# Kernel optimization log

Hardware: AMD Instinct MI355X
Metric: run time of the kernel (lower is better)

Reference implementation:

```python
import jax, jax.numpy as jnp
import numpy as np

N_HEADS = 16
HEAD_SIZE = 64
SEQ_LEN = 2048
EMBED = 1024
BATCH = 2


def setup_inputs() -> dict:
    key = jax.random.key(0)
    ks = jax.random.split(key, 9)
    d_inner = N_HEADS * HEAD_SIZE
    s = 1.0 / np.sqrt(EMBED)
    inp = {
        "inputs": jax.random.normal(ks[0], (BATCH, SEQ_LEN, EMBED), jnp.float32),
        "Wq": jax.random.uniform(ks[1], (EMBED, d_inner), jnp.float32, -s, s),
        "bq": jax.random.uniform(ks[2], (d_inner,), jnp.float32, -s, s),
        "Wk": jax.random.uniform(ks[3], (EMBED, d_inner), jnp.float32, -s, s),
        "bk": jax.random.uniform(ks[4], (d_inner,), jnp.float32, -s, s),
        "Wv": jax.random.uniform(ks[5], (EMBED, d_inner), jnp.float32, -s, s),
        "bv": jax.random.uniform(ks[6], (d_inner,), jnp.float32, -s, s),
        "Wo": jax.random.uniform(ks[7], (d_inner, EMBED), jnp.float32, -s, s),
        "bo": jax.random.uniform(ks[8], (EMBED,), jnp.float32, -s, s),
    }
    return inp


def reference(inputs, Wq, bq, Wk, bk, Wv, bv, Wo, bo):
    B, S, _ = inputs.shape
    # QKV projections -> [B, H, S, Dh]
    def proj(W, b):
        return (inputs @ W + b).reshape(B, S, N_HEADS, HEAD_SIZE).transpose(0, 2, 1, 3)
    q, k, v = proj(Wq, bq), proj(Wk, bk), proj(Wv, bv)
    scores = jnp.einsum("bhqd,bhkd->bhqk", q, k) / jnp.sqrt(jnp.float32(HEAD_SIZE))
    causal = jnp.tril(jnp.ones((S, S), dtype=bool))  # [S, S]
    scores = jnp.where(causal[None, None], scores, -jnp.inf)
    attn = jax.nn.softmax(scores, axis=-1)  # dropout is identity in eval
    out = jnp.einsum("bhqk,bhkd->bhqd", attn, v)
    out = out.transpose(0, 2, 1, 3).reshape(B, S, N_HEADS * HEAD_SIZE)
    return out @ Wo + bo
```

## Files before the change

### kernel.cpp

```cpp
#include <hip/hip_runtime.h>
#include <hip/hip_bf16.h>
#include <math.h>

#define NH 16
#define DH 64
#define SEQ 2048
#define EMBED 1024
#define DINNER 1024
#define BATCH 2
#define MTOK 4096

typedef __bf16 bf16x8 __attribute__((ext_vector_type(8)));
typedef float  f32x4  __attribute__((ext_vector_type(4)));
typedef float  f32x16 __attribute__((ext_vector_type(16)));
typedef unsigned int u32;

__device__ __forceinline__ void gload16(const void* g, void* l) {
    __builtin_amdgcn_global_load_lds((const __attribute__((address_space(1))) void*)g,
                                     (__attribute__((address_space(3))) void*)l, 16, 0, 0);
}

__global__ __launch_bounds__(256) void cvt_bf16(
    const float* __restrict__ src, __bf16* __restrict__ dst, int n)
{
    int i = (blockIdx.x * 256 + threadIdx.x) * 4;
    if (i + 3 < n) {
        float4 v = *(const float4*)&src[i];
        dst[i + 0] = (__bf16)v.x;
        dst[i + 1] = (__bf16)v.y;
        dst[i + 2] = (__bf16)v.z;
        dst[i + 3] = (__bf16)v.w;
    }
}

__global__ __launch_bounds__(256) void tconv4(
    const float* __restrict__ W0, const float* __restrict__ W1,
    const float* __restrict__ W2, const float* __restrict__ W3,
    __bf16* __restrict__ D0, __bf16* __restrict__ D1,
    __bf16* __restrict__ D2, __bf16* __restrict__ D3)
{
    const int z = blockIdx.z;
    const float* __restrict__ src = (z == 0) ? W0 : (z == 1) ? W1 : (z == 2) ? W2 : W3;
    __bf16* __restrict__ dst      = (z == 0) ? D0 : (z == 1) ? D1 : (z == 2) ? D2 : D3;
    const int R = 1024, C = 1024;

    __shared__ float t[32][33];
    const int c0 = blockIdx.x * 32, r0 = blockIdx.y * 32;
    const int x = threadIdx.x & 31, y = threadIdx.x >> 5;
#pragma unroll
    for (int i = 0; i < 4; ++i)
        t[y + 8 * i][x] = src[(size_t)(r0 + y + 8 * i) * C + c0 + x];
    __syncthreads();
#pragma unroll
    for (int i = 0; i < 4; ++i)
        dst[(size_t)(c0 + y + 8 * i) * R + r0 + x] = (__bf16)t[x][y + 8 * i];
}

#define QSCALE 0.18033688f

__global__ __launch_bounds__(256) void gemm128(
    const __bf16* __restrict__ A,
    const __bf16* __restrict__ Bt0, const __bf16* __restrict__ Bt1, const __bf16* __restrict__ Bt2,
    const float* __restrict__ b0, const float* __restrict__ b1, const float* __restrict__ b2,
    void* __restrict__ o0, void* __restrict__ o1, void* __restrict__ o2,
    int Kdim, int mode3)
{
    const int z = blockIdx.z;
    const __bf16* __restrict__ Bt = (z == 0) ? Bt0 : (z == 1) ? Bt1 : Bt2;
    const float*  __restrict__ bias = (z == 0) ? b0 : (z == 1) ? b1 : b2;
    void* __restrict__ outp = (z == 0) ? o0 : (z == 1) ? o1 : o2;
    const int mode = mode3 ? 3 : z;
    const float scale = (mode == 0) ? QSCALE : 1.0f;

    __shared__ __bf16 As[128 * 32];
    __shared__ __bf16 Bs[128 * 32];

    const int tid  = threadIdx.x;
    const int lane = tid & 63;
    const int wid  = tid >> 6;
    const int wm = wid >> 1, wn = wid & 1;
    const int ls = lane & 15, lg = lane >> 4;
    const int m0 = blockIdx.y * 128, n0 = blockIdx.x * 128;

    const int sr = tid >> 2;
    const int sc = (tid & 3) * 8;

    f32x4 acc[4][4] = {};

    for (int k0 = 0; k0 < Kdim; k0 += 32) {
        gload16(&A [(size_t)(m0 + sr)      * Kdim + k0 + sc], &As[sr * 32 + sc]);
        gload16(&A [(size_t)(m0 + 64 + sr) * Kdim + k0 + sc], &As[(64 + sr) * 32 + sc]);
        gload16(&Bt[(size_t)(n0 + sr)      * Kdim + k0 + sc], &Bs[sr * 32 + sc]);
        gload16(&Bt[(size_t)(n0 + 64 + sr) * Kdim + k0 + sc], &Bs[(64 + sr) * 32 + sc]);
        __syncthreads();

        bf16x8 af[4], bfr[4];
#pragma unroll
        for (int i = 0; i < 4; ++i) {
            af[i]  = *(const bf16x8*)&As[(wm * 64 + i * 16 + ls) * 32 + lg * 8];
            bfr[i] = *(const bf16x8*)&Bs[(wn * 64 + i * 16 + ls) * 32 + lg * 8];
        }
#pragma unroll
        for (int i = 0; i < 4; ++i)
#pragma unroll
            for (int jx = 0; jx < 4; ++jx)
                acc[i][jx] = __builtin_amdgcn_mfma_f32_16x16x32_bf16(af[i], bfr[jx], acc[i][jx], 0, 0, 0);
        __syncthreads();
    }

#pragma unroll
    for (int i = 0; i < 4; ++i) {
#pragma unroll
        for (int jx = 0; jx < 4; ++jx) {
#pragma unroll
            for (int j = 0; j < 4; ++j) {
                const int m = m0 + wm * 64 + i * 16 + lg * 4 + j;
                const int n = n0 + wn * 64 + jx * 16 + ls;
                const float v = (acc[i][jx][j] + bias[n]) * scale;
                if (mode == 3) {
                    ((float*)outp)[(size_t)m * EMBED + n] = v;
                } else {
                    const int b = m >> 11, s = m & 2047;
                    const int h = n >> 6,  d = n & 63;
                    if (mode == 2)
                        ((__bf16*)outp)[(((size_t)(b * NH + h) * DH + d) << 11) + s] = (__bf16)v;
                    else
                        ((__bf16*)outp)[((((size_t)(b * NH + h) << 11) + s) * DH) + d] = (__bf16)v;
                }
            }
        }
    }
}

__global__ __launch_bounds__(128) void attn_mfma(
    const __bf16* __restrict__ Q, const __bf16* __restrict__ K,
    const __bf16* __restrict__ Vt, __bf16* __restrict__ ctx)
{
    __shared__ __bf16 lds[2][8192];

    const int tid  = threadIdx.x;
    const int wave = tid >> 6;
    const int lane = tid & 63;
    const int col  = lane & 31;
    const int hi   = lane >> 5;
    const int bh = blockIdx.x & 31;
    const int qt = 31 - (blockIdx.x >> 5);
    const int qb  = qt * 64;
    const int qlo = qb + wave * 32;
    const int b = bh >> 4, h = bh & 15;

    const __bf16* __restrict__ Qb = Q + ((size_t)bh << 11) * DH;
    const char* __restrict__ Kg = (const char*)(K  + ((size_t)bh << 11) * DH);
    const char* __restrict__ Vg = (const char*)(Vt + ((size_t)bh << 11) * DH);

    const int srow = tid >> 3;
    const int sswz = ((tid & 7) * 16) ^ ((srow & 7) << 4);

    bf16x8 qf[4];
#pragma unroll
    for (int c = 0; c < 4; ++c)
        qf[c] = *(const bf16x8*)&Qb[(size_t)(qlo + col) * DH + c * 16 + hi * 8];

    const int nt = qt + 1;

#pragma unroll
    for (int i = 0; i < 4; ++i) {
        const int row = i * 16 + srow;
        gload16(Kg + (size_t)row * 128 + sswz,
                (char*)&lds[0][0] + i * 2048 + tid * 16);
        gload16(Vg + (size_t)row * 4096 + sswz,
                (char*)&lds[0][0] + 8192 + i * 2048 + tid * 16);
    }
    __syncthreads();

    f32x16 oT0 = {}, oT1 = {};
    float mrun = -INFINITY, lrun = 0.f;
    int cur = 0;
    const int swz = (col & 7) << 4;

    for (int t = 0; t < nt; ++t) {
        if (t + 1 < nt) {
            const int kbn = (t + 1) * 64;
#pragma unroll
            for (int i = 0; i < 4; ++i) {
                const int row = i * 16 + srow;
                gload16(Kg + (size_t)(kbn + row) * 128 + sswz,
                        (char*)&lds[cur ^ 1][0] + i * 2048 + tid * 16);
                gload16(Vg + (size_t)row * 4096 + (size_t)kbn * 2 + sswz,
                        (char*)&lds[cur ^ 1][0] + 8192 + i * 2048 + tid * 16);
            }
        }

        const int k0 = t * 64;
        const char* ldsK = (const char*)&lds[cur][0];
        const char* ldsV = ldsK + 8192;

        bf16x8 kfa[4], kfb[4];
#pragma unroll
        for (int c = 0; c < 4; ++c) {
            kfa[c] = *(const bf16x8*)(ldsK + (     col) * 128 + ((c * 32 + hi * 16) ^ swz));
            kfb[c] = *(const bf16x8*)(ldsK + (32 + col) * 128 + ((c * 32 + hi * 16) ^ swz));
        }

        f32x16 sta = {}, stb = {};
#pragma unroll
        for (int c = 0; c < 4; ++c) {
            sta = __builtin_amdgcn_mfma_f32_32x32x16_bf16(kfa[c], qf[c], sta, 0, 0, 0);
            stb = __builtin_amdgcn_mfma_f32_32x32x16_bf16(kfb[c], qf[c], stb, 0, 0, 0);
        }

        if (k0 + 63 > qlo) {
#pragma unroll
            for (int r = 0; r < 16; ++r) {
                const int krel = (r & 3) + 8 * (r >> 2) + 4 * hi;
                if (k0 + krel > qlo + col)      sta[r] = -INFINITY;
                if (k0 + 32 + krel > qlo + col) stb[r] = -INFINITY;
            }
        }

        float ta = fmaxf(fmaxf(fmaxf(sta[0], sta[1]), fmaxf(sta[2], sta[3])),
                         fmaxf(fmaxf(sta[4], sta[5]), fmaxf(sta[6], sta[7])));
        float tb = fmaxf(fmaxf(fmaxf(sta[8], sta[9]),  fmaxf(sta[10], sta[11])),
                         fmaxf(fmaxf(sta[12], sta[13]), fmaxf(sta[14], sta[15])));
        float tc = fmaxf(fmaxf(fmaxf(stb[0], stb[1]), fmaxf(stb[2], stb[3])),
                         fmaxf(fmaxf(stb[4], stb[5]), fmaxf(stb[6], stb[7])));
        float td = fmaxf(fmaxf(fmaxf(stb[8], stb[9]),  fmaxf(stb[10], stb[11])),
                         fmaxf(fmaxf(stb[12], stb[13]), fmaxf(stb[14], stb[15])));
        float tmax = fmaxf(fmaxf(ta, tb), fmaxf(tc, td));
        tmax = fmaxf(tmax, __shfl_xor(tmax, 32));

        if (__any(tmax > mrun + 8.f)) {
            const float mnew = fmaxf(mrun, tmax);
            const float corr = exp2f(mrun - mnew);
            lrun *= corr;
            oT0 *= corr;
            oT1 *= corr;
            mrun = mnew;
        }

        float pa[16], pb[16];
#pragma unroll
        for (int r = 0; r < 16; ++r) { pa[r] = exp2f(sta[r] - mrun); pb[r] = exp2f(stb[r] - mrun); }
        float psa = (((pa[0] + pa[1]) + (pa[2] + pa[3])) + ((pa[4] + pa[5]) + (pa[6] + pa[7])))
                  + (((pa[8] + pa[9]) + (pa[10] + pa[11])) + ((pa[12] + pa[13]) + (pa[14] + pa[15])));
        float psb = (((pb[0] + pb[1]) + (pb[2] + pb[3])) + ((pb[4] + pb[5]) + (pb[6] + pb[7])))
                  + (((pb[8] + pb[9]) + (pb[10] + pb[11])) + ((pb[12] + pb[13]) + (pb[14] + pb[15])));
        float psum = psa + psb;
        psum += __shfl_xor(psum, 32);
        lrun += psum;

        u32 wa[8], wb[8];
#pragma unroll
        for (int i = 0; i < 8; ++i) {
            u32 r1, r2;
            asm("v_cvt_pk_bf16_f32 %0, %1, %2" : "=v"(r1) : "v"(pa[2 * i]), "v"(pa[2 * i + 1]));
            asm("v_cvt_pk_bf16_f32 %0, %1, %2" : "=v"(r2) : "v"(pb[2 * i]), "v"(pb[2 * i + 1]));
            wa[i] = r1; wb[i] = r2;
        }
        asm("v_permlane32_swap_b32 %0, %1" : "+v"(wa[0]), "+v"(wa[2]));
        asm("v_permlane32_swap_b32 %0, %1" : "+v"(wa[1]), "+v"(wa[3]));
        asm("v_permlane32_swap_b32 %0, %1" : "+v"(wa[4]), "+v"(wa[6]));
        asm("v_permlane32_swap_b32 %0, %1" : "+v"(wa[5]), "+v"(wa[7]));
        asm("v_permlane32_swap_b32 %0, %1" : "+v"(wb[0]), "+v"(wb[2]));
        asm("v_permlane32_swap_b32 %0, %1" : "+v"(wb[1]), "+v"(wb[3]));
        asm("v_permlane32_swap_b32 %0, %1" : "+v"(wb[4]), "+v"(wb[6]));
        asm("v_permlane32_swap_b32 %0, %1" : "+v"(wb[5]), "+v"(wb[7]));

        union { u32 u[4]; bf16x8 v; } cA0, cA1, cB0, cB1;
        cA0.u[0] = wa[0]; cA0.u[1] = wa[1]; cA0.u[2] = wa[2]; cA0.u[3] = wa[3];
        cA1.u[0] = wa[4]; cA1.u[1] = wa[5]; cA1.u[2] = wa[6]; cA1.u[3] = wa[7];
        cB0.u[0] = wb[0]; cB0.u[1] = wb[1]; cB0.u[2] = wb[2]; cB0.u[3] = wb[3];
        cB1.u[0] = wb[4]; cB1.u[1] = wb[5]; cB1.u[2] = wb[6]; cB1.u[3] = wb[7];

#pragma unroll
        for (int dh = 0; dh < 2; ++dh) {
            bf16x8 v0 = *(const bf16x8*)(ldsV + (dh * 32 + col) * 128 + ((0  + hi * 16) ^ swz));
            bf16x8 v1 = *(const bf16x8*)(ldsV + (dh * 32 + col) * 128 + ((32 + hi * 16) ^ swz));
            bf16x8 v2 = *(const bf16x8*)(ldsV + (dh * 32 + col) * 128 + ((64 + hi * 16) ^ swz));
            bf16x8 v3 = *(const bf16x8*)(ldsV + (dh * 32 + col) * 128 + ((96 + hi * 16) ^ swz));
            f32x16& o = dh ? oT1 : oT0;
            o = __builtin_amdgcn_mfma_f32_32x32x16_bf16(v0, cA0.v, o, 0, 0, 0);
            o = __builtin_amdgcn_mfma_f32_32x32x16_bf16(v1, cA1.v, o, 0, 0, 0);
            o = __builtin_amdgcn_mfma_f32_32x32x16_bf16(v2, cB0.v, o, 0, 0, 0);
            o = __builtin_amdgcn_mfma_f32_32x32x16_bf16(v3, cB1.v, o, 0, 0, 0);
        }

        __syncthreads();
        cur ^= 1;
    }

    const float inv = 1.0f / lrun;
    const size_t base = ((size_t)(b * SEQ + qlo + col)) * DINNER + h * 64;
#pragma unroll
    for (int g = 0; g < 4; ++g) {
        __bf16 t4[4];
#pragma unroll
        for (int j = 0; j < 4; ++j) t4[j] = (__bf16)(oT0[4 * g + j] * inv);
        *(uint2*)&ctx[base + 8 * g + 4 * hi] = *(uint2*)t4;
#pragma unroll
        for (int j = 0; j < 4; ++j) t4[j] = (__bf16)(oT1[4 * g + j] * inv);
        *(uint2*)&ctx[base + 32 + 8 * g + 4 * hi] = *(uint2*)t4;
    }
}

extern "C" void kernel_launch(void* const* d_in, const int* in_sizes, int n_in,
                              void* d_out, int out_size, void* d_ws, size_t ws_size,
                              hipStream_t stream)
{
    const float* X  = (const float*)d_in[0];
    const float* Wq = (const float*)d_in[1];
    const float* bq = (const float*)d_in[2];
    const float* Wk = (const float*)d_in[3];
    const float* bk = (const float*)d_in[4];
    const float* Wv = (const float*)d_in[5];
    const float* bv = (const float*)d_in[6];
    const float* Wo = (const float*)d_in[7];
    const float* bo = (const float*)d_in[8];
    float* out = (float*)d_out;

    __bf16* ws  = (__bf16*)d_ws;
    const size_t MI = 1048576;
    __bf16* Xb   = ws;
    __bf16* Wtq  = ws + 4  * MI;
    __bf16* Wtk  = ws + 5  * MI;
    __bf16* Wtv  = ws + 6  * MI;
    __bf16* Wto  = ws + 7  * MI;
    __bf16* Qb   = ws + 8  * MI;
    __bf16* Kb   = ws + 12 * MI;
    __bf16* Vtb  = ws + 16 * MI;
    __bf16* ctxb = ws + 20 * MI;

    cvt_bf16<<<dim3(MTOK * EMBED / 1024), dim3(256), 0, stream>>>(X, Xb, MTOK * EMBED);
    tconv4<<<dim3(32, 32, 4), dim3(256), 0, stream>>>(Wq, Wk, Wv, Wo, Wtq, Wtk, Wtv, Wto);

    {
        dim3 grid(DINNER / 128, MTOK / 128, 3), blk(256);
        gemm128<<<grid, blk, 0, stream>>>(Xb, Wtq, Wtk, Wtv, bq, bk, bv,
                                          Qb, Kb, Vtb, EMBED, 0);
    }

    {
        dim3 grid(32 * (SEQ / 64)), blk(128);
        attn_mfma<<<grid, blk, 0, stream>>>(Qb, Kb, Vtb, ctxb);
    }

    {
        dim3 grid(EMBED / 128, MTOK / 128, 1), blk(256);
        gemm128<<<grid, blk, 0, stream>>>(ctxb, Wto, Wto, Wto, bo, bo, bo,
                                          out, out, out, DINNER, 1);
    }
}
```

Before: 150.3 us.

## Split attention KV loop across two waves per 32-row query tile

Each block now handles a 32-row query tile instead of 64, and its two waves take alternating 64-key tiles of the causal KV range (split-K). At the end, the two waves' partial softmax states are merged through LDS using max/sum rescaling. The grid doubles to raise parallelism and balance work across the causal triangle. In exchange, K/V tiles are loaded per block for only 32 queries, which halves data reuse, and there is an extra LDS merge and sync while one wave sits idle during each tile.

```diff
diff --git a/kernel.cpp b/kernel.cpp
--- a/kernel.cpp
+++ b/kernel.cpp
@@ -143,10 +143,9 @@
     const int lane = tid & 63;
     const int col  = lane & 31;
     const int hi   = lane >> 5;
-    const int bh = blockIdx.x & 31;
-    const int qt = 31 - (blockIdx.x >> 5);
-    const int qb  = qt * 64;
-    const int qlo = qb + wave * 32;
+    const int bh   = blockIdx.x & 31;
+    const int qt32 = 63 - (blockIdx.x >> 5);
+    const int qlo  = qt32 * 32;
     const int b = bh >> 4, h = bh & 15;
 
     const __bf16* __restrict__ Qb = Q + ((size_t)bh << 11) * DH;
@@ -155,13 +154,14 @@
 
     const int srow = tid >> 3;
     const int sswz = ((tid & 7) * 16) ^ ((srow & 7) << 4);
+    const int swz  = (col & 7) << 4;
 
     bf16x8 qf[4];
 #pragma unroll
     for (int c = 0; c < 4; ++c)
         qf[c] = *(const bf16x8*)&Qb[(size_t)(qlo + col) * DH + c * 16 + hi * 8];
 
-    const int nt = qt + 1;
+    const int nt = (qt32 + 2) >> 1;
 
 #pragma unroll
     for (int i = 0; i < 4; ++i) {
@@ -176,7 +176,6 @@
     f32x16 oT0 = {}, oT1 = {};
     float mrun = -INFINITY, lrun = 0.f;
     int cur = 0;
-    const int swz = (col & 7) << 4;
 
     for (int t = 0; t < nt; ++t) {
         if (t + 1 < nt) {
@@ -191,115 +190,137 @@
             }
         }
 
-        const int k0 = t * 64;
-        const char* ldsK = (const char*)&lds[cur][0];
-        const char* ldsV = ldsK + 8192;
-
-        bf16x8 kfa[4], kfb[4];
-#pragma unroll
-        for (int c = 0; c < 4; ++c) {
-            kfa[c] = *(const bf16x8*)(ldsK + (     col) * 128 + ((c * 32 + hi * 16) ^ swz));
-            kfb[c] = *(const bf16x8*)(ldsK + (32 + col) * 128 + ((c * 32 + hi * 16) ^ swz));
-        }
-
-        f32x16 sta = {}, stb = {};
-#pragma unroll
-        for (int c = 0; c < 4; ++c) {
-            sta = __builtin_amdgcn_mfma_f32_32x32x16_bf16(kfa[c], qf[c], sta, 0, 0, 0);
-            stb = __builtin_amdgcn_mfma_f32_32x32x16_bf16(kfb[c], qf[c], stb, 0, 0, 0);
-        }
-
-        if (k0 + 63 > qlo) {
-#pragma unroll
-            for (int r = 0; r < 16; ++r) {
-                const int krel = (r & 3) + 8 * (r >> 2) + 4 * hi;
-                if (k0 + krel > qlo + col)      sta[r] = -INFINITY;
-                if (k0 + 32 + krel > qlo + col) stb[r] = -INFINITY;
-            }
-        }
-
-        float ta = fmaxf(fmaxf(fmaxf(sta[0], sta[1]), fmaxf(sta[2], sta[3])),
-                         fmaxf(fmaxf(sta[4], sta[5]), fmaxf(sta[6], sta[7])));
-        float tb = fmaxf(fmaxf(fmaxf(sta[8], sta[9]),  fmaxf(sta[10], sta[11])),
-                         fmaxf(fmaxf(sta[12], sta[13]), fmaxf(sta[14], sta[15])));
-        float tc = fmaxf(fmaxf(fmaxf(stb[0], stb[1]), fmaxf(stb[2], stb[3])),
-                         fmaxf(fmaxf(stb[4], stb[5]), fmaxf(stb[6], stb[7])));
-        float td = fmaxf(fmaxf(fmaxf(stb[8], stb[9]),  fmaxf(stb[10], stb[11])),
-                         fmaxf(fmaxf(stb[12], stb[13]), fmaxf(stb[14], stb[15])));
-        float tmax = fmaxf(fmaxf(ta, tb), fmaxf(tc, td));
-        tmax = fmaxf(tmax, __shfl_xor(tmax, 32));
-
-        if (__any(tmax > mrun + 8.f)) {
-            const float mnew = fmaxf(mrun, tmax);
-            const float corr = exp2f(mrun - mnew);
-            lrun *= corr;
-            oT0 *= corr;
-            oT1 *= corr;
-            mrun = mnew;
-        }
-
-        float pa[16], pb[16];
-#pragma unroll
-        for (int r = 0; r < 16; ++r) { pa[r] = exp2f(sta[r] - mrun); pb[r] = exp2f(stb[r] - mrun); }
-        float psa = (((pa[0] + pa[1]) + (pa[2] + pa[3])) + ((pa[4] + pa[5]) + (pa[6] + pa[7])))
-                  + (((pa[8] + pa[9]) + (pa[10] + pa[11])) + ((pa[12] + pa[13]) + (pa[14] + pa[15])));
-        float psb = (((pb[0] + pb[1]) + (pb[2] + pb[3])) + ((pb[4] + pb[5]) + (pb[6] + pb[7])))
-                  + (((pb[8] + pb[9]) + (pb[10] + pb[11])) + ((pb[12] + pb[13]) + (pb[14] + pb[15])));
-        float psum = psa + psb;
-        psum += __shfl_xor(psum, 32);
-        lrun += psum;
-
-        u32 wa[8], wb[8];
-#pragma unroll
-        for (int i = 0; i < 8; ++i) {
-            u32 r1, r2;
-            asm("v_cvt_pk_bf16_f32 %0, %1, %2" : "=v"(r1) : "v"(pa[2 * i]), "v"(pa[2 * i + 1]));
-            asm("v_cvt_pk_bf16_f32 %0, %1, %2" : "=v"(r2) : "v"(pb[2 * i]), "v"(pb[2 * i + 1]));
-            wa[i] = r1; wb[i] = r2;
-        }
-        asm("v_permlane32_swap_b32 %0, %1" : "+v"(wa[0]), "+v"(wa[2]));
-        asm("v_permlane32_swap_b32 %0, %1" : "+v"(wa[1]), "+v"(wa[3]));
-        asm("v_permlane32_swap_b32 %0, %1" : "+v"(wa[4]), "+v"(wa[6]));
-        asm("v_permlane32_swap_b32 %0, %1" : "+v"(wa[5]), "+v"(wa[7]));
-        asm("v_permlane32_swap_b32 %0, %1" : "+v"(wb[0]), "+v"(wb[2]));
-        asm("v_permlane32_swap_b32 %0, %1" : "+v"(wb[1]), "+v"(wb[3]));
-        asm("v_permlane32_swap_b32 %0, %1" : "+v"(wb[4]), "+v"(wb[6]));
-        asm("v_permlane32_swap_b32 %0, %1" : "+v"(wb[5]), "+v"(wb[7]));
-
-        union { u32 u[4]; bf16x8 v; } cA0, cA1, cB0, cB1;
-        cA0.u[0] = wa[0]; cA0.u[1] = wa[1]; cA0.u[2] = wa[2]; cA0.u[3] = wa[3];
-        cA1.u[0] = wa[4]; cA1.u[1] = wa[5]; cA1.u[2] = wa[6]; cA1.u[3] = wa[7];
-        cB0.u[0] = wb[0]; cB0.u[1] = wb[1]; cB0.u[2] = wb[2]; cB0.u[3] = wb[3];
-        cB1.u[0] = wb[4]; cB1.u[1] = wb[5]; cB1.u[2] = wb[6]; cB1.u[3] = wb[7];
-
-#pragma unroll
-        for (int dh = 0; dh < 2; ++dh) {
-            bf16x8 v0 = *(const bf16x8*)(ldsV + (dh * 32 + col) * 128 + ((0  + hi * 16) ^ swz));
-            bf16x8 v1 = *(const bf16x8*)(ldsV + (dh * 32 + col) * 128 + ((32 + hi * 16) ^ swz));
-            bf16x8 v2 = *(const bf16x8*)(ldsV + (dh * 32 + col) * 128 + ((64 + hi * 16) ^ swz));
-            bf16x8 v3 = *(const bf16x8*)(ldsV + (dh * 32 + col) * 128 + ((96 + hi * 16) ^ swz));
-            f32x16& o = dh ? oT1 : oT0;
-            o = __builtin_amdgcn_mfma_f32_32x32x16_bf16(v0, cA0.v, o, 0, 0, 0);
-            o = __builtin_amdgcn_mfma_f32_32x32x16_bf16(v1, cA1.v, o, 0, 0, 0);
-            o = __builtin_amdgcn_mfma_f32_32x32x16_bf16(v2, cB0.v, o, 0, 0, 0);
-            o = __builtin_amdgcn_mfma_f32_32x32x16_bf16(v3, cB1.v, o, 0, 0, 0);
+        if ((t & 1) == wave) {
+            const int k0 = t * 64;
+            const char* ldsK = (const char*)&lds[cur][0];
+            const char* ldsV = ldsK + 8192;
+
+            bf16x8 kfa[4], kfb[4];
+#pragma unroll
+            for (int c = 0; c < 4; ++c) {
+                kfa[c] = *(const bf16x8*)(ldsK + (     col) * 128 + ((c * 32 + hi * 16) ^ swz));
+                kfb[c] = *(const bf16x8*)(ldsK + (32 + col) * 128 + ((c * 32 + hi * 16) ^ swz));
+            }
+
+            f32x16 sta = {}, stb = {};
+#pragma unroll
+            for (int c = 0; c < 4; ++c) {
+                sta = __builtin_amdgcn_mfma_f32_32x32x16_bf16(kfa[c], qf[c], sta, 0, 0, 0);
+                stb = __builtin_amdgcn_mfma_f32_32x32x16_bf16(kfb[c], qf[c], stb, 0, 0, 0);
+            }
+
+            if (k0 + 63 > qlo) {
+#pragma unroll
+                for (int r = 0; r < 16; ++r) {
+                    const int krel = (r & 3) + 8 * (r >> 2) + 4 * hi;
+                    if (k0 + krel > qlo + col)      sta[r] = -INFINITY;
+                    if (k0 + 32 + krel > qlo + col) stb[r] = -INFINITY;
+                }
+            }
+
+            float ta = fmaxf(fmaxf(fmaxf(sta[0], sta[1]), fmaxf(sta[2], sta[3])),
+                             fmaxf(fmaxf(sta[4], sta[5]), fmaxf(sta[6], sta[7])));
+            float tb = fmaxf(fmaxf(fmaxf(sta[8], sta[9]),  fmaxf(sta[10], sta[11])),
+                             fmaxf(fmaxf(sta[12], sta[13]), fmaxf(sta[14], sta[15])));
+            float tc = fmaxf(fmaxf(fmaxf(stb[0], stb[1]), fmaxf(stb[2], stb[3])),
+                             fmaxf(fmaxf(stb[4], stb[5]), fmaxf(stb[6], stb[7])));
+            float td = fmaxf(fmaxf(fmaxf(stb[8], stb[9]),  fmaxf(stb[10], stb[11])),
+                             fmaxf(fmaxf(stb[12], stb[13]), fmaxf(stb[14], stb[15])));
+            float tmax = fmaxf(fmaxf(ta, tb), fmaxf(tc, td));
+            tmax = fmaxf(tmax, __shfl_xor(tmax, 32));
+
+            if (__any(tmax > mrun + 8.f)) {
+                const float mnew = fmaxf(mrun, tmax);
+                const float corr = exp2f(mrun - mnew);
+                lrun *= corr;
+                oT0 *= corr;
+                oT1 *= corr;
+                mrun = mnew;
+            }
+
+            float pa[16], pb[16];
+#pragma unroll
+            for (int r = 0; r < 16; ++r) { pa[r] = exp2f(sta[r] - mrun); pb[r] = exp2f(stb[r] - mrun); }
+            float psa = (((pa[0] + pa[1]) + (pa[2] + pa[3])) + ((pa[4] + pa[5]) + (pa[6] + pa[7])))
+                      + (((pa[8] + pa[9]) + (pa[10] + pa[11])) + ((pa[12] + pa[13]) + (pa[14] + pa[15])));
+            float psb = (((pb[0] + pb[1]) + (pb[2] + pb[3])) + ((pb[4] + pb[5]) + (pb[6] + pb[7])))
+                      + (((pb[8] + pb[9]) + (pb[10] + pb[11])) + ((pb[12] + pb[13]) + (pb[14] + pb[15])));
+            float psum = psa + psb;
+            psum += __shfl_xor(psum, 32);
+            lrun += psum;
+
+            u32 wa[8], wb[8];
+#pragma unroll
+            for (int i = 0; i < 8; ++i) {
+                u32 r1, r2;
+                asm("v_cvt_pk_bf16_f32 %0, %1, %2" : "=v"(r1) : "v"(pa[2 * i]), "v"(pa[2 * i + 1]));
+                asm("v_cvt_pk_bf16_f32 %0, %1, %2" : "=v"(r2) : "v"(pb[2 * i]), "v"(pb[2 * i + 1]));
+                wa[i] = r1; wb[i] = r2;
+            }
+            asm("v_permlane32_swap_b32 %0, %1" : "+v"(wa[0]), "+v"(wa[2]));
+            asm("v_permlane32_swap_b32 %0, %1" : "+v"(wa[1]), "+v"(wa[3]));
+            asm("v_permlane32_swap_b32 %0, %1" : "+v"(wa[4]), "+v"(wa[6]));
+            asm("v_permlane32_swap_b32 %0, %1" : "+v"(wa[5]), "+v"(wa[7]));
+            asm("v_permlane32_swap_b32 %0, %1" : "+v"(wb[0]), "+v"(wb[2]));
+            asm("v_permlane32_swap_b32 %0, %1" : "+v"(wb[1]), "+v"(wb[3]));
+            asm("v_permlane32_swap_b32 %0, %1" : "+v"(wb[4]), "+v"(wb[6]));
+            asm("v_permlane32_swap_b32 %0, %1" : "+v"(wb[5]), "+v"(wb[7]));
+
+            union { u32 u4[4]; bf16x8 v; } cA0, cA1, cB0, cB1;
+            cA0.u4[0] = wa[0]; cA0.u4[1] = wa[1]; cA0.u4[2] = wa[2]; cA0.u4[3] = wa[3];
+            cA1.u4[0] = wa[4]; cA1.u4[1] = wa[5]; cA1.u4[2] = wa[6]; cA1.u4[3] = wa[7];
+            cB0.u4[0] = wb[0]; cB0.u4[1] = wb[1]; cB0.u4[2] = wb[2]; cB0.u4[3] = wb[3];
+            cB1.u4[0] = wb[4]; cB1.u4[1] = wb[5]; cB1.u4[2] = wb[6]; cB1.u4[3] = wb[7];
+
+#pragma unroll
+            for (int dh = 0; dh < 2; ++dh) {
+                bf16x8 v0 = *(const bf16x8*)(ldsV + (dh * 32 + col) * 128 + ((0  + hi * 16) ^ swz));
+                bf16x8 v1 = *(const bf16x8*)(ldsV + (dh * 32 + col) * 128 + ((32 + hi * 16) ^ swz));
+                bf16x8 v2 = *(const bf16x8*)(ldsV + (dh * 32 + col) * 128 + ((64 + hi * 16) ^ swz));
+                bf16x8 v3 = *(const bf16x8*)(ldsV + (dh * 32 + col) * 128 + ((96 + hi * 16) ^ swz));
+                f32x16& o = dh ? oT1 : oT0;
+                o = __builtin_amdgcn_mfma_f32_32x32x16_bf16(v0, cA0.v, o, 0, 0, 0);
+                o = __builtin_amdgcn_mfma_f32_32x32x16_bf16(v1, cA1.v, o, 0, 0, 0);
+                o = __builtin_amdgcn_mfma_f32_32x32x16_bf16(v2, cB0.v, o, 0, 0, 0);
+                o = __builtin_amdgcn_mfma_f32_32x32x16_bf16(v3, cB1.v, o, 0, 0, 0);
+            }
         }
 
         __syncthreads();
         cur ^= 1;
     }
 
-    const float inv = 1.0f / lrun;
-    const size_t base = ((size_t)(b * SEQ + qlo + col)) * DINNER + h * 64;
-#pragma unroll
-    for (int g = 0; g < 4; ++g) {
-        __bf16 t4[4];
-#pragma unroll
-        for (int j = 0; j < 4; ++j) t4[j] = (__bf16)(oT0[4 * g + j] * inv);
-        *(uint2*)&ctx[base + 8 * g + 4 * hi] = *(uint2*)t4;
-#pragma unroll
-        for (int j = 0; j < 4; ++j) t4[j] = (__bf16)(oT1[4 * g + j] * inv);
-        *(uint2*)&ctx[base + 32 + 8 * g + 4 * hi] = *(uint2*)t4;
+    float* mrg = (float*)&lds[0][0];
+    if (wave == 1) {
+#pragma unroll
+        for (int r = 0; r < 16; ++r) {
+            mrg[r * 64 + lane]        = oT0[r];
+            mrg[(16 + r) * 64 + lane] = oT1[r];
+        }
+        mrg[32 * 64 + lane] = mrun;
+        mrg[33 * 64 + lane] = lrun;
+    }
+    __syncthreads();
+    if (wave == 0) {
+        const float m1 = mrg[32 * 64 + lane];
+        const float l1 = mrg[33 * 64 + lane];
+        const float M  = fmaxf(mrun, m1);
+        const float c0 = exp2f(mrun - M);
+        const float c1 = (m1 == -INFINITY) ? 0.f : exp2f(m1 - M);
+        const float inv = 1.0f / (lrun * c0 + l1 * c1);
+        const size_t base = ((size_t)(b * SEQ + qlo + col)) * DINNER + h * 64;
+#pragma unroll
+        for (int g = 0; g < 4; ++g) {
+            __bf16 t4[4];
+#pragma unroll
+            for (int j = 0; j < 4; ++j)
+                t4[j] = (__bf16)((oT0[4 * g + j] * c0 + mrg[(4 * g + j) * 64 + lane] * c1) * inv);
+            *(uint2*)&ctx[base + 8 * g + 4 * hi] = *(uint2*)t4;
+#pragma unroll
+            for (int j = 0; j < 4; ++j)
+                t4[j] = (__bf16)((oT1[4 * g + j] * c0 + mrg[(16 + 4 * g + j) * 64 + lane] * c1) * inv);
+            *(uint2*)&ctx[base + 32 + 8 * g + 4 * hi] = *(uint2*)t4;
+        }
     }
 }
 
@@ -340,7 +361,7 @@
     }
 
     {
-        dim3 grid(32 * (SEQ / 64)), blk(128);
+        dim3 grid(32 * (SEQ / 32)), blk(128);
         attn_mfma<<<grid, blk, 0, stream>>>(Qb, Kb, Vtb, ctxb);
     }
 
```

Result: no change. 151.6 us (+0.9%).

## Use single-wave attention blocks with split K/V single-buffer prefetch and waitcnt sync

Applied to the files above, without the earlier changes.

Each attention workgroup now holds one wave covering 32 queries instead of two waves covering 64, which doubles the grid and removes __syncthreads. The double-buffered LDS is replaced by a single buffer. The next K tile is prefetched after the QK MFMAs and the next V tile after the PV MFMAs, with explicit vmcnt/lgkmcnt waits and setprio around the MFMA sections. This aims to cut LDS use and barrier cost and improve occupancy. In exchange, each wave now loads its own K/V tiles, so global traffic for the same keys roughly doubles, and the prefetch window is shorter.

```diff
diff --git a/kernel.cpp b/kernel.cpp
--- a/kernel.cpp
+++ b/kernel.cpp
@@ -132,68 +132,52 @@
     }
 }
 
-__global__ __launch_bounds__(128) void attn_mfma(
+__global__ __launch_bounds__(64) void attn_mfma(
     const __bf16* __restrict__ Q, const __bf16* __restrict__ K,
     const __bf16* __restrict__ Vt, __bf16* __restrict__ ctx)
 {
-    __shared__ __bf16 lds[2][8192];
-
-    const int tid  = threadIdx.x;
-    const int wave = tid >> 6;
-    const int lane = tid & 63;
+    __shared__ __bf16 lds[8192];
+
+    const int lane = threadIdx.x & 63;
     const int col  = lane & 31;
     const int hi   = lane >> 5;
-    const int bh = blockIdx.x & 31;
-    const int qt = 31 - (blockIdx.x >> 5);
-    const int qb  = qt * 64;
-    const int qlo = qb + wave * 32;
+    const int bh   = blockIdx.x & 31;
+    const int qt32 = 63 - (blockIdx.x >> 5);
+    const int qlo  = qt32 * 32;
     const int b = bh >> 4, h = bh & 15;
 
     const __bf16* __restrict__ Qb = Q + ((size_t)bh << 11) * DH;
     const char* __restrict__ Kg = (const char*)(K  + ((size_t)bh << 11) * DH);
     const char* __restrict__ Vg = (const char*)(Vt + ((size_t)bh << 11) * DH);
 
-    const int srow = tid >> 3;
-    const int sswz = ((tid & 7) * 16) ^ ((srow & 7) << 4);
+    char* ldsK = (char*)&lds[0];
+    char* ldsV = ldsK + 8192;
+
+    const int srow = lane >> 3;
+    const int sswz = ((lane & 7) * 16) ^ (srow << 4);
+    const int swz  = (col & 7) << 4;
 
     bf16x8 qf[4];
 #pragma unroll
     for (int c = 0; c < 4; ++c)
         qf[c] = *(const bf16x8*)&Qb[(size_t)(qlo + col) * DH + c * 16 + hi * 8];
 
-    const int nt = qt + 1;
-
-#pragma unroll
-    for (int i = 0; i < 4; ++i) {
-        const int row = i * 16 + srow;
-        gload16(Kg + (size_t)row * 128 + sswz,
-                (char*)&lds[0][0] + i * 2048 + tid * 16);
-        gload16(Vg + (size_t)row * 4096 + sswz,
-                (char*)&lds[0][0] + 8192 + i * 2048 + tid * 16);
-    }
-    __syncthreads();
+    const int nt = (qt32 + 2) >> 1;
+
+#pragma unroll
+    for (int i = 0; i < 8; ++i)
+        gload16(Kg + (size_t)(i * 8 + srow) * 128 + sswz, ldsK + i * 1024 + lane * 16);
+#pragma unroll
+    for (int i = 0; i < 8; ++i)
+        gload16(Vg + (size_t)(i * 8 + srow) * 4096 + sswz, ldsV + i * 1024 + lane * 16);
 
     f32x16 oT0 = {}, oT1 = {};
     float mrun = -INFINITY, lrun = 0.f;
-    int cur = 0;
-    const int swz = (col & 7) << 4;
 
     for (int t = 0; t < nt; ++t) {
-        if (t + 1 < nt) {
-            const int kbn = (t + 1) * 64;
-#pragma unroll
-            for (int i = 0; i < 4; ++i) {
-                const int row = i * 16 + srow;
-                gload16(Kg + (size_t)(kbn + row) * 128 + sswz,
-                        (char*)&lds[cur ^ 1][0] + i * 2048 + tid * 16);
-                gload16(Vg + (size_t)row * 4096 + (size_t)kbn * 2 + sswz,
-                        (char*)&lds[cur ^ 1][0] + 8192 + i * 2048 + tid * 16);
-            }
-        }
-
         const int k0 = t * 64;
-        const char* ldsK = (const char*)&lds[cur][0];
-        const char* ldsV = ldsK + 8192;
+
+        asm volatile("s_waitcnt vmcnt(8)" ::: "memory");
 
         bf16x8 kfa[4], kfb[4];
 #pragma unroll
@@ -202,11 +186,23 @@
             kfb[c] = *(const bf16x8*)(ldsK + (32 + col) * 128 + ((c * 32 + hi * 16) ^ swz));
         }
 
+        __builtin_amdgcn_s_setprio(1);
         f32x16 sta = {}, stb = {};
 #pragma unroll
         for (int c = 0; c < 4; ++c) {
             sta = __builtin_amdgcn_mfma_f32_32x32x16_bf16(kfa[c], qf[c], sta, 0, 0, 0);
             stb = __builtin_amdgcn_mfma_f32_32x32x16_bf16(kfb[c], qf[c], stb, 0, 0, 0);
+        }
+        __builtin_amdgcn_s_setprio(0);
+
+        asm volatile("s_waitcnt lgkmcnt(0)" ::: "memory");
+        __builtin_amdgcn_sched_barrier(0);
+        if (t + 1 < nt) {
+            const int kbn = (t + 1) * 64;
+#pragma unroll
+            for (int i = 0; i < 8; ++i)
+                gload16(Kg + (size_t)(kbn + i * 8 + srow) * 128 + sswz,
+                        ldsK + i * 1024 + lane * 16);
         }
 
         if (k0 + 63 > qlo) {
@@ -266,12 +262,16 @@
         asm("v_permlane32_swap_b32 %0, %1" : "+v"(wb[4]), "+v"(wb[6]));
         asm("v_permlane32_swap_b32 %0, %1" : "+v"(wb[5]), "+v"(wb[7]));
 
-        union { u32 u[4]; bf16x8 v; } cA0, cA1, cB0, cB1;
-        cA0.u[0] = wa[0]; cA0.u[1] = wa[1]; cA0.u[2] = wa[2]; cA0.u[3] = wa[3];
-        cA1.u[0] = wa[4]; cA1.u[1] = wa[5]; cA1.u[2] = wa[6]; cA1.u[3] = wa[7];
-        cB0.u[0] = wb[0]; cB0.u[1] = wb[1]; cB0.u[2] = wb[2]; cB0.u[3] = wb[3];
-        cB1.u[0] = wb[4]; cB1.u[1] = wb[5]; cB1.u[2] = wb[6]; cB1.u[3] = wb[7];
-
+        union { u32 u4[4]; bf16x8 v; } cA0, cA1, cB0, cB1;
+        cA0.u4[0] = wa[0]; cA0.u4[1] = wa[1]; cA0.u4[2] = wa[2]; cA0.u4[3] = wa[3];
+        cA1.u4[0] = wa[4]; cA1.u4[1] = wa[5]; cA1.u4[2] = wa[6]; cA1.u4[3] = wa[7];
+        cB0.u4[0] = wb[0]; cB0.u4[1] = wb[1]; cB0.u4[2] = wb[2]; cB0.u4[3] = wb[3];
+        cB1.u4[0] = wb[4]; cB1.u4[1] = wb[5]; cB1.u4[2] = wb[6]; cB1.u4[3] = wb[7];
+
+        if (t + 1 < nt) { asm volatile("s_waitcnt vmcnt(8)" ::: "memory"); }
+        else            { asm volatile("s_waitcnt vmcnt(0)" ::: "memory"); }
+
+        __builtin_amdgcn_s_setprio(1);
 #pragma unroll
         for (int dh = 0; dh < 2; ++dh) {
             bf16x8 v0 = *(const bf16x8*)(ldsV + (dh * 32 + col) * 128 + ((0  + hi * 16) ^ swz));
@@ -284,9 +284,17 @@
             o = __builtin_amdgcn_mfma_f32_32x32x16_bf16(v2, cB0.v, o, 0, 0, 0);
             o = __builtin_amdgcn_mfma_f32_32x32x16_bf16(v3, cB1.v, o, 0, 0, 0);
         }
-
-        __syncthreads();
-        cur ^= 1;
+        __builtin_amdgcn_s_setprio(0);
+
+        asm volatile("s_waitcnt lgkmcnt(0)" ::: "memory");
+        __builtin_amdgcn_sched_barrier(0);
+        if (t + 1 < nt) {
+            const int kbn = (t + 1) * 64;
+#pragma unroll
+            for (int i = 0; i < 8; ++i)
+                gload16(Vg + (size_t)(i * 8 + srow) * 4096 + (size_t)kbn * 2 + sswz,
+                        ldsV + i * 1024 + lane * 16);
+        }
     }
 
     const float inv = 1.0f / lrun;
@@ -340,7 +348,7 @@
     }
 
     {
-        dim3 grid(32 * (SEQ / 64)), blk(128);
+        dim3 grid(32 * (SEQ / 32)), blk(64);
         attn_mfma<<<grid, blk, 0, stream>>>(Qb, Kb, Vtb, ctxb);
     }
 
```

After: 145.3 us. 1.03x faster.
